# Optimization experiments

Hardware: AMD Instinct MI355X
Metric: run time of the kernel (lower is better)

Reference implementation:

```python
import jax, jax.numpy as jnp
import numpy as np

H = 8          # num_heads
WIN = 63       # win_size
LEFT = WIN - 1 - WIN // 2  # 31
EPS = 1e-5


def layer_norm(x, w, b):
    mu = x.mean(-1, keepdims=True)
    var = ((x - mu) ** 2).mean(-1, keepdims=True)
    return (x - mu) / jnp.sqrt(var + EPS) * w + b


def setup_inputs() -> dict:
    key = jax.random.key(0)
    N, T, C = 2, 2048, 512
    hid = 4 * C
    ks = jax.random.split(key, 16)
    s = 0.02
    return {
        "x": jax.random.normal(ks[0], (N, T, C), jnp.float32),
        "norm1_w": jnp.ones((C,), jnp.float32),
        "norm1_b": jnp.zeros((C,), jnp.float32),
        "qkv_w": jax.random.normal(ks[1], (3 * C, C), jnp.float32) * s,
        "qkv_b": jnp.zeros((3 * C,), jnp.float32),
        "rel_bias": jax.random.normal(ks[2], (H, WIN), jnp.float32) * s,
        "proj_w": jax.random.normal(ks[3], (C, C), jnp.float32) * s,
        "proj_b": jnp.zeros((C,), jnp.float32),
        "norm2_w": jnp.ones((C,), jnp.float32),
        "norm2_b": jnp.zeros((C,), jnp.float32),
        "fc1_w": jax.random.normal(ks[4], (hid, C), jnp.float32) * s,
        "fc1_b": jnp.zeros((hid,), jnp.float32),
        "fc2_w": jax.random.normal(ks[5], (C, hid), jnp.float32) * s,
        "fc2_b": jnp.zeros((C,), jnp.float32),
    }


def reference(x, norm1_w, norm1_b, qkv_w, qkv_b, rel_bias, proj_w, proj_b,
              norm2_w, norm2_b, fc1_w, fc1_b, fc2_w, fc2_b):
    N, T, C = x.shape
    hd = C // H
    scale = hd ** -0.5
    right = WIN - LEFT - 1

    shortcut = x
    h = layer_norm(x, norm1_w, norm1_b)
    qkv = (h @ qkv_w.T + qkv_b).reshape(N, T, 3, H, hd)
    q, k, v = qkv[:, :, 0], qkv[:, :, 1], qkv[:, :, 2]  # (N,T,H,hd)

    # zero-pad keys/values along time, gather sliding windows
    kp = jnp.pad(k, ((0, 0), (LEFT, right), (0, 0), (0, 0)))
    vp = jnp.pad(v, ((0, 0), (LEFT, right), (0, 0), (0, 0)))
    idx = jnp.arange(T)[:, None] + jnp.arange(WIN)[None, :]
    k_win = kp[:, idx]
    v_win = vp[:, idx]

    attn = jnp.einsum('nthd,ntwhd->nhtw', q * scale, k_win)
    attn = attn + rel_bias[None, :, None, :]
    # boundary mask: key position j = t - LEFT + w must lie in [0, T)
    pos = idx - LEFT
    mask = jnp.where((pos < 0) | (pos >= T), jnp.float32(-100.0), jnp.float32(0.0))
    attn = attn + mask[None, None, :, :]
    attn = jax.nn.softmax(attn, axis=-1)

    out = jnp.einsum('nhtw,ntwhd->nthd', attn, v_win).reshape(N, T, C)
    out = out @ proj_w.T + proj_b

    x = shortcut + out
    h2 = layer_norm(x, norm2_w, norm2_b)
    m = jax.nn.gelu(h2 @ fc1_w.T + fc1_b, approximate=False)  # torch nn.GELU = exact erf
    m = m @ fc2_w.T + fc2_b
    return x + m
```

## Files before the change

### kernel.cpp

```cpp
#include <hip/hip_runtime.h>

typedef unsigned short u16;
typedef unsigned int uint;
typedef __attribute__((ext_vector_type(4))) float floatx4;
typedef __attribute__((ext_vector_type(16))) float floatx16;
typedef __attribute__((ext_vector_type(8))) short shortx8;

__device__ __forceinline__ u16 f2b(float f) {
    unsigned int u = __float_as_uint(f);
    unsigned int r = (u + 0x7fffu + ((u >> 16) & 1u)) >> 16;
    return (u16)r;
}
__device__ __forceinline__ float b2f(u16 u) {
    return __uint_as_float(((unsigned int)u) << 16);
}
__device__ __forceinline__ void gl_lds16(const u16* g, u16* l) {
    __builtin_amdgcn_global_load_lds(
        (const __attribute__((address_space(1))) void*)g,
        (__attribute__((address_space(3))) void*)l, 16, 0, 0);
}
__device__ __forceinline__ float gelu_f(float v) {
    float e = __expf(1.59576912f * v * (1.0f + 0.044715f * v * v));
    return v * e / (e + 1.0f);
}

__device__ __forceinline__ void ln_row(const float* __restrict__ x,
                                       const float* __restrict__ w,
                                       const float* __restrict__ b,
                                       u16* __restrict__ out, int row,
                                       float* red) {
    const float2* xr = (const float2*)(x + (size_t)row * 512);
    float2 v = xr[threadIdx.x];
    float s = v.x + v.y;
    float s2 = v.x * v.x + v.y * v.y;
    #pragma unroll
    for (int o = 32; o > 0; o >>= 1) {
        s += __shfl_down(s, o, 64);
        s2 += __shfl_down(s2, o, 64);
    }
    int wid = threadIdx.x >> 6, lane = threadIdx.x & 63;
    if (lane == 0) { red[wid] = s; red[4 + wid] = s2; }
    __syncthreads();
    s = red[0] + red[1] + red[2] + red[3];
    s2 = red[4] + red[5] + red[6] + red[7];
    float mu = s * (1.0f / 512.0f);
    float var = s2 * (1.0f / 512.0f) - mu * mu;
    float rstd = rsqrtf(var + 1e-5f);
    float2 wv = ((const float2*)w)[threadIdx.x];
    float2 bv = ((const float2*)b)[threadIdx.x];
    float o0 = (v.x - mu) * rstd * wv.x + bv.x;
    float o1 = (v.y - mu) * rstd * wv.y + bv.y;
    unsigned int pack = (unsigned)f2b(o0) | ((unsigned)f2b(o1) << 16);
    ((unsigned int*)(out + (size_t)row * 512))[threadIdx.x] = pack;
}

__global__ __launch_bounds__(256) void ln_kernel_b(const u16* __restrict__ x,
                                                   const float* __restrict__ w,
                                                   const float* __restrict__ b,
                                                   u16* __restrict__ out) {
    __shared__ float red[8];
    int row = blockIdx.x;
    uint pv = ((const uint*)(x + (size_t)row * 512))[threadIdx.x];
    float vx = b2f((u16)(pv & 0xffffu)), vy = b2f((u16)(pv >> 16));
    float s = vx + vy;
    float s2 = vx * vx + vy * vy;
    #pragma unroll
    for (int o = 32; o > 0; o >>= 1) {
        s += __shfl_down(s, o, 64);
        s2 += __shfl_down(s2, o, 64);
    }
    int wid = threadIdx.x >> 6, lane = threadIdx.x & 63;
    if (lane == 0) { red[wid] = s; red[4 + wid] = s2; }
    __syncthreads();
    s = red[0] + red[1] + red[2] + red[3];
    s2 = red[4] + red[5] + red[6] + red[7];
    float mu = s * (1.0f / 512.0f);
    float var = s2 * (1.0f / 512.0f) - mu * mu;
    float rstd = rsqrtf(var + 1e-5f);
    float2 wv = ((const float2*)w)[threadIdx.x];
    float2 bv = ((const float2*)b)[threadIdx.x];
    float o0 = (vx - mu) * rstd * wv.x + bv.x;
    float o1 = (vy - mu) * rstd * wv.y + bv.y;
    unsigned int pack = (unsigned)f2b(o0) | ((unsigned)f2b(o1) << 16);
    ((unsigned int*)(out + (size_t)row * 512))[threadIdx.x] = pack;
}

__global__ __launch_bounds__(256) void prep_kernel(
    const float* __restrict__ qkvw, u16* __restrict__ wq,
    const float* __restrict__ projw, u16* __restrict__ wp,
    const float* __restrict__ fc1w, u16* __restrict__ w1,
    const float* __restrict__ fc2w, u16* __restrict__ w2,
    const float* __restrict__ x, const float* __restrict__ n1w,
    const float* __restrict__ n1b, u16* __restrict__ hb) {
    __shared__ float red[8];
    int bi = blockIdx.x;
    if (bi < 3072) {
        const float* src;
        u16* dst;
        int i0;
        if (bi < 768)       { src = qkvw; dst = wq; i0 = bi; }
        else if (bi < 1024) { src = projw; dst = wp; i0 = bi - 768; }
        else if (bi < 2048) { src = fc1w; dst = w1; i0 = bi - 1024; }
        else                { src = fc2w; dst = w2; i0 = bi - 2048; }
        int i = i0 * 256 + threadIdx.x;
        float4 v = ((const float4*)src)[i];
        uint2 o;
        o.x = (unsigned)f2b(v.x) | ((unsigned)f2b(v.y) << 16);
        o.y = (unsigned)f2b(v.z) | ((unsigned)f2b(v.w) << 16);
        ((uint2*)dst)[i] = o;
    } else {
        ln_row(x, n1w, n1b, hb, bi - 3072, red);
    }
}

template <int BM, int BN, int BK, int EPI>
__global__ __launch_bounds__(256, 2) void gemm_lds(const u16* __restrict__ A,
                                                   const u16* __restrict__ W,
                                                   const float* __restrict__ bias,
                                                   const float* __restrict__ residF,
                                                   const u16* __restrict__ residB,
                                                   float* __restrict__ outF,
                                                   u16* __restrict__ outB,
                                                   int M, int Nn, int K) {
    constexpr int MI = BM / 2 / 32;
    constexpr int NI = BN / 2 / 32;
    constexpr int CPR = BK / 8;
    constexpr int KMSK = CPR - 1;
    constexpr int ACH = BM * CPR / 256;
    constexpr int BCH = BN * CPR / 256;
    __shared__ u16 a_s[2][BM * BK];
    __shared__ u16 b_s[2][BN * BK];

    int tid = threadIdx.x;
    int wid = tid >> 6, lane = tid & 63;
    int wm = wid >> 1, wn = wid & 1;
    int m_blk = blockIdx.y * BM;
    int n_blk = blockIdx.x * BN;
    int lr = lane & 31;
    int lk = lane >> 5;

    floatx16 acc[MI][NI];
    #pragma unroll
    for (int i = 0; i < MI; i++)
        #pragma unroll
        for (int j = 0; j < NI; j++)
            #pragma unroll
            for (int r = 0; r < 16; r++) acc[i][j][r] = 0.f;

    const u16* Ag = A + (size_t)m_blk * K;
    const u16* Wg = W + (size_t)n_blk * K;

    int arow[ACH], akc[ACH], brow[BCH], bkc[BCH];
    #pragma unroll
    for (int p = 0; p < ACH; p++) {
        int c = p * 256 + tid;
        arow[p] = c / CPR;
        akc[p] = (c & KMSK) ^ (arow[p] & KMSK);
    }
    #pragma unroll
    for (int p = 0; p < BCH; p++) {
        int c = p * 256 + tid;
        brow[p] = c / CPR;
        bkc[p] = (c & KMSK) ^ (brow[p] & KMSK);
    }

    auto stage = [&](int k0, int buf) {
        #pragma unroll
        for (int p = 0; p < ACH; p++)
            gl_lds16(Ag + (size_t)arow[p] * K + k0 + akc[p] * 8,
                     a_s[buf] + (p * 256 + tid) * 8);
        #pragma unroll
        for (int p = 0; p < BCH; p++)
            gl_lds16(Wg + (size_t)brow[p] * K + k0 + bkc[p] * 8,
                     b_s[buf] + (p * 256 + tid) * 8);
    };

    stage(0, 0);
    int nit = K / BK;
    for (int it = 0; it < nit; it++) {
        __syncthreads();
        if (it + 1 < nit) stage((it + 1) * BK, (it + 1) & 1);
        int cb = it & 1;
        #pragma unroll
        for (int s = 0; s < BK / 16; s++) {
            shortx8 af[MI], bf[NI];
            int kc = s * 2 + lk;
            #pragma unroll
            for (int i = 0; i < MI; i++) {
                int row = wm * (BM / 2) + i * 32 + lr;
                af[i] = *(const shortx8*)(a_s[cb] + (row * CPR + (kc ^ (row & KMSK))) * 8);
            }
            #pragma unroll
            for (int j = 0; j < NI; j++) {
                int row = wn * (BN / 2) + j * 32 + lr;
                bf[j] = *(const shortx8*)(b_s[cb] + (row * CPR + (kc ^ (row & KMSK))) * 8);
            }
            #pragma unroll
            for (int i = 0; i < MI; i++)
                #pragma unroll
                for (int j = 0; j < NI; j++)
                    acc[i][j] = __builtin_amdgcn_mfma_f32_32x32x16_bf16(
                        af[i], bf[j], acc[i][j], 0, 0, 0);
        }
    }

    int col_l = lane & 31;
    int row_q = 4 * (lane >> 5);
    #pragma unroll
    for (int nj = 0; nj < NI; nj++) {
        int col = n_blk + wn * (BN / 2) + nj * 32 + col_l;
        float bv = bias[col];
        #pragma unroll
        for (int mi = 0; mi < MI; mi++) {
            #pragma unroll
            for (int r = 0; r < 16; r++) {
                int row = m_blk + wm * (BM / 2) + mi * 32 + (r & 3) + 8 * (r >> 2) + row_q;
                size_t off = (size_t)row * Nn + col;
                float v = acc[mi][nj][r] + bv;
                if (EPI == 1) {
                    outB[off] = f2b(v + residF[off]);
                } else if (EPI == 2) {
                    outB[off] = f2b(gelu_f(v));
                } else if (EPI == 3) {
                    outF[off] = v + b2f(residB[off]);
                } else {
                    outB[off] = f2b(v);
                }
            }
        }
    }
}

__global__ __launch_bounds__(256) void attn_kernel(const u16* __restrict__ qkv,
                                                   const float* __restrict__ rel_bias,
                                                   u16* __restrict__ out) {
    __shared__ u16 k_s[128][72];
    __shared__ u16 v_t[64][152];
    __shared__ u16 p_s[4][16][104];
    __shared__ float s_bias[64];

    int bx = blockIdx.x;
    int n = bx >> 8;
    int h = (bx >> 5) & 7;
    int t0 = (bx & 31) << 6;
    int tid = threadIdx.x, wid = tid >> 6, lane = tid & 63;
    int col = lane & 15, rq = lane >> 4;

    const u16* qrow = qkv + (size_t)(n * 2048 + t0 + wid * 16 + col) * 1536 + h * 64 + rq * 8;
    shortx8 qf0 = *(const shortx8*)qrow;
    shortx8 qf1 = *(const shortx8*)(qrow + 32);

    if (tid < 63) s_bias[tid] = rel_bias[h * 63 + tid];
    if (tid == 63) s_bias[63] = 0.f;

    const uint* qkv_u = (const uint*)qkv;
    for (int idx = tid; idx < 128 * 32; idx += 256) {
        int row = idx >> 5, j = idx & 31;
        int pos = t0 - 31 + row;
        uint kv = 0;
        if (pos >= 0 && pos < 2048)
            kv = qkv_u[(size_t)(n * 2048 + pos) * 768 + 256 + h * 32 + j];
        *(uint*)&k_s[row][j * 2] = kv;
    }
    for (int idx = tid; idx < 144 * 32; idx += 256) {
        int row = idx >> 5, j = idx & 31;
        int pos = t0 - 31 + row;
        uint vv = 0;
        if (pos >= 0 && pos < 2048)
            vv = qkv_u[(size_t)(n * 2048 + pos) * 768 + 512 + h * 32 + j];
        v_t[2 * j][row] = (u16)(vv & 0xffffu);
        v_t[2 * j + 1][row] = (u16)(vv >> 16);
    }
    __syncthreads();

    floatx4 S[5];
    #pragma unroll
    for (int nt = 0; nt < 5; nt++) S[nt] = (floatx4){0.f, 0.f, 0.f, 0.f};
    #pragma unroll
    for (int nt = 0; nt < 5; nt++) {
        const u16* kb = &k_s[wid * 16 + nt * 16 + col][rq * 8];
        shortx8 b0 = *(const shortx8*)kb;
        shortx8 b1 = *(const shortx8*)(kb + 32);
        S[nt] = __builtin_amdgcn_mfma_f32_16x16x32_bf16(qf0, b0, S[nt], 0, 0, 0);
        S[nt] = __builtin_amdgcn_mfma_f32_16x16x32_bf16(qf1, b1, S[nt], 0, 0, 0);
    }

    #pragma unroll
    for (int r = 0; r < 4; r++) {
        int t_row = rq * 4 + r;
        float sc[5];
        float mx = -1e30f;
        #pragma unroll
        for (int nt = 0; nt < 5; nt++) {
            int w = nt * 16 + col - t_row;
            int pos_abs = t0 - 31 + wid * 16 + nt * 16 + col;
            float v;
            if (w < 0 || w > 62) {
                v = -1e30f;
            } else {
                v = S[nt][r] * 0.125f + s_bias[w];
                if (pos_abs < 0 || pos_abs >= 2048) v -= 100.f;
            }
            sc[nt] = v;
            mx = fmaxf(mx, v);
        }
        #pragma unroll
        for (int o = 1; o < 16; o <<= 1) mx = fmaxf(mx, __shfl_xor(mx, o, 64));
        float l = 0.f;
        #pragma unroll
        for (int nt = 0; nt < 5; nt++) {
            sc[nt] = __expf(sc[nt] - mx);
            l += sc[nt];
        }
        #pragma unroll
        for (int o = 1; o < 16; o <<= 1) l += __shfl_xor(l, o, 64);
        float inv = 1.0f / l;
        #pragma unroll
        for (int nt = 0; nt < 5; nt++)
            p_s[wid][t_row][nt * 16 + col] = f2b(sc[nt] * inv);
        p_s[wid][t_row][80 + col] = 0;
    }
    __syncthreads();

    floatx4 O[4];
    #pragma unroll
    for (int dt = 0; dt < 4; dt++) O[dt] = (floatx4){0.f, 0.f, 0.f, 0.f};
    const u16* pr = &p_s[wid][col][rq * 8];
    shortx8 a0 = *(const shortx8*)pr;
    shortx8 a1 = *(const shortx8*)(pr + 32);
    shortx8 a2 = *(const shortx8*)(pr + 64);
    #pragma unroll
    for (int dt = 0; dt < 4; dt++) {
        const u16* vb = &v_t[dt * 16 + col][wid * 16 + rq * 8];
        shortx8 b0 = *(const shortx8*)vb;
        shortx8 b1 = *(const shortx8*)(vb + 32);
        shortx8 b2 = *(const shortx8*)(vb + 64);
        O[dt] = __builtin_amdgcn_mfma_f32_16x16x32_bf16(a0, b0, O[dt], 0, 0, 0);
        O[dt] = __builtin_amdgcn_mfma_f32_16x16x32_bf16(a1, b1, O[dt], 0, 0, 0);
        O[dt] = __builtin_amdgcn_mfma_f32_16x16x32_bf16(a2, b2, O[dt], 0, 0, 0);
    }

    #pragma unroll
    for (int dt = 0; dt < 4; dt++) {
        #pragma unroll
        for (int r = 0; r < 4; r++) {
            int t_row = rq * 4 + r;
            out[(size_t)(n * 2048 + t0 + wid * 16 + t_row) * 512 + h * 64 + dt * 16 + col] =
                f2b(O[dt][r]);
        }
    }
}

extern "C" void kernel_launch(void* const* d_in, const int* in_sizes, int n_in,
                              void* d_out, int out_size, void* d_ws, size_t ws_size,
                              hipStream_t stream) {
    const float* x     = (const float*)d_in[0];
    const float* n1w   = (const float*)d_in[1];
    const float* n1b   = (const float*)d_in[2];
    const float* qkvw  = (const float*)d_in[3];
    const float* qkvbv = (const float*)d_in[4];
    const float* relb  = (const float*)d_in[5];
    const float* projw = (const float*)d_in[6];
    const float* projb = (const float*)d_in[7];
    const float* n2w   = (const float*)d_in[8];
    const float* n2b   = (const float*)d_in[9];
    const float* fc1w  = (const float*)d_in[10];
    const float* fc1b  = (const float*)d_in[11];
    const float* fc2w  = (const float*)d_in[12];
    const float* fc2b  = (const float*)d_in[13];
    float* out = (float*)d_out;

    char* p = (char*)d_ws;
    u16* wq   = (u16*)p;  p += (size_t)786432 * 2;
    u16* wp   = (u16*)p;  p += (size_t)262144 * 2;
    u16* w1   = (u16*)p;  p += (size_t)1048576 * 2;
    u16* w2   = (u16*)p;  p += (size_t)1048576 * 2;
    u16* hb   = (u16*)p;  p += (size_t)2097152 * 2;
    u16* qkvb = (u16*)p;  p += (size_t)6291456 * 2;
    u16* attb = (u16*)p;  p += (size_t)2097152 * 2;
    u16* x2b  = (u16*)p;  p += (size_t)2097152 * 2;
    u16* mb   = (u16*)p;  p += (size_t)8388608 * 2;

    prep_kernel<<<7168, 256, 0, stream>>>(qkvw, wq, projw, wp, fc1w, w1, fc2w, w2,
                                          x, n1w, n1b, hb);
    gemm_lds<128, 128, 64, 0><<<dim3(12, 32), 256, 0, stream>>>(
        hb, wq, qkvbv, nullptr, nullptr, nullptr, qkvb, 4096, 1536, 512);
    attn_kernel<<<512, 256, 0, stream>>>(qkvb, relb, attb);
    gemm_lds<64, 64, 128, 1><<<dim3(8, 64), 256, 0, stream>>>(
        attb, wp, projb, x, nullptr, nullptr, x2b, 4096, 512, 512);
    ln_kernel_b<<<4096, 256, 0, stream>>>(x2b, n2w, n2b, hb);
    gemm_lds<128, 128, 64, 2><<<dim3(16, 32), 256, 0, stream>>>(
        hb, w1, fc1b, nullptr, nullptr, nullptr, mb, 4096, 2048, 512);
    gemm_lds<64, 64, 128, 3><<<dim3(8, 64), 256, 0, stream>>>(
        mb, w2, fc2b, nullptr, x2b, out, nullptr, 4096, 512, 2048);
}
```

Before: 177.8 us.

## Use wave-per-row layernorm and split GEMMs into 16x16 and 32x32 MFMA variants

Layernorm kernels now process one row per wavefront with 128-bit loads and xor-shuffle reductions, which removes the LDS reduction and block barrier and cuts the block count. The large GEMMs (QKV, FC1) move to a dedicated kernel using 16x16x32 MFMA with a 4x4 accumulator tile per wave. The small-N GEMMs (proj, FC2) get a specialised single 32x32 accumulator kernel. Grid axes are swapped so consecutive blocks walk along M, which changes how blocks share weight tiles in cache.

Measured after the change: 167.6 us, median of 2. 5.7% less time.

```diff
diff --git a/kernel.cpp b/kernel.cpp
--- a/kernel.cpp
+++ b/kernel.cpp
@@ -24,65 +24,82 @@
     return v * e / (e + 1.0f);
 }
 
-__device__ __forceinline__ void ln_row(const float* __restrict__ x,
-                                       const float* __restrict__ w,
-                                       const float* __restrict__ b,
-                                       u16* __restrict__ out, int row,
-                                       float* red) {
-    const float2* xr = (const float2*)(x + (size_t)row * 512);
-    float2 v = xr[threadIdx.x];
-    float s = v.x + v.y;
-    float s2 = v.x * v.x + v.y * v.y;
+__device__ __forceinline__ void ln_row_wave_f32(const float* __restrict__ x,
+                                                const float* __restrict__ w,
+                                                const float* __restrict__ b,
+                                                u16* __restrict__ out, int row) {
+    int lane = threadIdx.x & 63;
+    const float4* xr = (const float4*)(x + (size_t)row * 512);
+    float4 v0 = xr[lane * 2], v1 = xr[lane * 2 + 1];
+    float s = v0.x + v0.y + v0.z + v0.w + v1.x + v1.y + v1.z + v1.w;
+    float s2 = v0.x * v0.x + v0.y * v0.y + v0.z * v0.z + v0.w * v0.w +
+               v1.x * v1.x + v1.y * v1.y + v1.z * v1.z + v1.w * v1.w;
     #pragma unroll
     for (int o = 32; o > 0; o >>= 1) {
-        s += __shfl_down(s, o, 64);
-        s2 += __shfl_down(s2, o, 64);
-    }
-    int wid = threadIdx.x >> 6, lane = threadIdx.x & 63;
-    if (lane == 0) { red[wid] = s; red[4 + wid] = s2; }
-    __syncthreads();
-    s = red[0] + red[1] + red[2] + red[3];
-    s2 = red[4] + red[5] + red[6] + red[7];
+        s += __shfl_xor(s, o, 64);
+        s2 += __shfl_xor(s2, o, 64);
+    }
     float mu = s * (1.0f / 512.0f);
     float var = s2 * (1.0f / 512.0f) - mu * mu;
     float rstd = rsqrtf(var + 1e-5f);
-    float2 wv = ((const float2*)w)[threadIdx.x];
-    float2 bv = ((const float2*)b)[threadIdx.x];
-    float o0 = (v.x - mu) * rstd * wv.x + bv.x;
-    float o1 = (v.y - mu) * rstd * wv.y + bv.y;
-    unsigned int pack = (unsigned)f2b(o0) | ((unsigned)f2b(o1) << 16);
-    ((unsigned int*)(out + (size_t)row * 512))[threadIdx.x] = pack;
+    const float4* wr = (const float4*)w;
+    const float4* br = (const float4*)b;
+    float4 w0 = wr[lane * 2], w1 = wr[lane * 2 + 1];
+    float4 b0 = br[lane * 2], b1 = br[lane * 2 + 1];
+    uint4 o4;
+    o4.x = (uint)f2b((v0.x - mu) * rstd * w0.x + b0.x) |
+           ((uint)f2b((v0.y - mu) * rstd * w0.y + b0.y) << 16);
+    o4.y = (uint)f2b((v0.z - mu) * rstd * w0.z + b0.z) |
+           ((uint)f2b((v0.w - mu) * rstd * w0.w + b0.w) << 16);
+    o4.z = (uint)f2b((v1.x - mu) * rstd * w1.x + b1.x) |
+           ((uint)f2b((v1.y - mu) * rstd * w1.y + b1.y) << 16);
+    o4.w = (uint)f2b((v1.z - mu) * rstd * w1.z + b1.z) |
+           ((uint)f2b((v1.w - mu) * rstd * w1.w + b1.w) << 16);
+    ((uint4*)(out + (size_t)row * 512))[lane] = o4;
 }
 
 __global__ __launch_bounds__(256) void ln_kernel_b(const u16* __restrict__ x,
                                                    const float* __restrict__ w,
                                                    const float* __restrict__ b,
                                                    u16* __restrict__ out) {
-    __shared__ float red[8];
-    int row = blockIdx.x;
-    uint pv = ((const uint*)(x + (size_t)row * 512))[threadIdx.x];
-    float vx = b2f((u16)(pv & 0xffffu)), vy = b2f((u16)(pv >> 16));
-    float s = vx + vy;
-    float s2 = vx * vx + vy * vy;
+    int row = blockIdx.x * 4 + (threadIdx.x >> 6);
+    int lane = threadIdx.x & 63;
+    uint4 p = ((const uint4*)(x + (size_t)row * 512))[lane];
+    float v[8];
+    v[0] = b2f((u16)(p.x & 0xffffu)); v[1] = b2f((u16)(p.x >> 16));
+    v[2] = b2f((u16)(p.y & 0xffffu)); v[3] = b2f((u16)(p.y >> 16));
+    v[4] = b2f((u16)(p.z & 0xffffu)); v[5] = b2f((u16)(p.z >> 16));
+    v[6] = b2f((u16)(p.w & 0xffffu)); v[7] = b2f((u16)(p.w >> 16));
+    float s = 0.f, s2 = 0.f;
+    #pragma unroll
+    for (int i = 0; i < 8; i++) { s += v[i]; s2 += v[i] * v[i]; }
     #pragma unroll
     for (int o = 32; o > 0; o >>= 1) {
-        s += __shfl_down(s, o, 64);
-        s2 += __shfl_down(s2, o, 64);
-    }
-    int wid = threadIdx.x >> 6, lane = threadIdx.x & 63;
-    if (lane == 0) { red[wid] = s; red[4 + wid] = s2; }
-    __syncthreads();
-    s = red[0] + red[1] + red[2] + red[3];
-    s2 = red[4] + red[5] + red[6] + red[7];
+        s += __shfl_xor(s, o, 64);
+        s2 += __shfl_xor(s2, o, 64);
+    }
     float mu = s * (1.0f / 512.0f);
     float var = s2 * (1.0f / 512.0f) - mu * mu;
     float rstd = rsqrtf(var + 1e-5f);
-    float2 wv = ((const float2*)w)[threadIdx.x];
-    float2 bv = ((const float2*)b)[threadIdx.x];
-    float o0 = (vx - mu) * rstd * wv.x + bv.x;
-    float o1 = (vy - mu) * rstd * wv.y + bv.y;
-    unsigned int pack = (unsigned)f2b(o0) | ((unsigned)f2b(o1) << 16);
-    ((unsigned int*)(out + (size_t)row * 512))[threadIdx.x] = pack;
+    const float4* wr = (const float4*)w;
+    const float4* br = (const float4*)b;
+    float4 w0 = wr[lane * 2], w1 = wr[lane * 2 + 1];
+    float4 b0 = br[lane * 2], b1 = br[lane * 2 + 1];
+    float o8[8];
+    o8[0] = (v[0] - mu) * rstd * w0.x + b0.x;
+    o8[1] = (v[1] - mu) * rstd * w0.y + b0.y;
+    o8[2] = (v[2] - mu) * rstd * w0.z + b0.z;
+    o8[3] = (v[3] - mu) * rstd * w0.w + b0.w;
+    o8[4] = (v[4] - mu) * rstd * w1.x + b1.x;
+    o8[5] = (v[5] - mu) * rstd * w1.y + b1.y;
+    o8[6] = (v[6] - mu) * rstd * w1.z + b1.z;
+    o8[7] = (v[7] - mu) * rstd * w1.w + b1.w;
+    uint4 o4;
+    o4.x = (uint)f2b(o8[0]) | ((uint)f2b(o8[1]) << 16);
+    o4.y = (uint)f2b(o8[2]) | ((uint)f2b(o8[3]) << 16);
+    o4.z = (uint)f2b(o8[4]) | ((uint)f2b(o8[5]) << 16);
+    o4.w = (uint)f2b(o8[6]) | ((uint)f2b(o8[7]) << 16);
+    ((uint4*)(out + (size_t)row * 512))[lane] = o4;
 }
 
 __global__ __launch_bounds__(256) void prep_kernel(
@@ -92,7 +109,6 @@
     const float* __restrict__ fc2w, u16* __restrict__ w2,
     const float* __restrict__ x, const float* __restrict__ n1w,
     const float* __restrict__ n1b, u16* __restrict__ hb) {
-    __shared__ float red[8];
     int bi = blockIdx.x;
     if (bi < 3072) {
         const float* src;
@@ -105,73 +121,144 @@
         int i = i0 * 256 + threadIdx.x;
         float4 v = ((const float4*)src)[i];
         uint2 o;
-        o.x = (unsigned)f2b(v.x) | ((unsigned)f2b(v.y) << 16);
-        o.y = (unsigned)f2b(v.z) | ((unsigned)f2b(v.w) << 16);
+        o.x = (uint)f2b(v.x) | ((uint)f2b(v.y) << 16);
+        o.y = (uint)f2b(v.z) | ((uint)f2b(v.w) << 16);
         ((uint2*)dst)[i] = o;
     } else {
-        ln_row(x, n1w, n1b, hb, bi - 3072, red);
-    }
-}
-
-template <int BM, int BN, int BK, int EPI>
-__global__ __launch_bounds__(256, 2) void gemm_lds(const u16* __restrict__ A,
-                                                   const u16* __restrict__ W,
-                                                   const float* __restrict__ bias,
-                                                   const float* __restrict__ residF,
-                                                   const u16* __restrict__ residB,
-                                                   float* __restrict__ outF,
-                                                   u16* __restrict__ outB,
-                                                   int M, int Nn, int K) {
-    constexpr int MI = BM / 2 / 32;
-    constexpr int NI = BN / 2 / 32;
-    constexpr int CPR = BK / 8;
-    constexpr int KMSK = CPR - 1;
-    constexpr int ACH = BM * CPR / 256;
-    constexpr int BCH = BN * CPR / 256;
+        int row = (bi - 3072) * 4 + (threadIdx.x >> 6);
+        ln_row_wave_f32(x, n1w, n1b, hb, row);
+    }
+}
+
+template <int EPI>
+__global__ __launch_bounds__(256, 2) void gemm16(const u16* __restrict__ A,
+                                                 const u16* __restrict__ W,
+                                                 const float* __restrict__ bias,
+                                                 u16* __restrict__ outB,
+                                                 int M, int Nn, int K) {
+    constexpr int BM = 128, BN = 128, BK = 64;
     __shared__ u16 a_s[2][BM * BK];
     __shared__ u16 b_s[2][BN * BK];
 
     int tid = threadIdx.x;
     int wid = tid >> 6, lane = tid & 63;
     int wm = wid >> 1, wn = wid & 1;
-    int m_blk = blockIdx.y * BM;
-    int n_blk = blockIdx.x * BN;
+    int m_blk = blockIdx.x * BM;
+    int n_blk = blockIdx.y * BN;
+    int lr = lane & 15;
+    int lkc = lane >> 4;
+
+    floatx4 acc[4][4];
+    #pragma unroll
+    for (int i = 0; i < 4; i++)
+        #pragma unroll
+        for (int j = 0; j < 4; j++) acc[i][j] = (floatx4){0.f, 0.f, 0.f, 0.f};
+
+    const u16* Ag = A + (size_t)m_blk * K;
+    const u16* Wg = W + (size_t)n_blk * K;
+
+    int srow = tid >> 3;
+    int skc = (tid & 7) ^ (srow & 7);
+
+    auto stage = [&](int k0, int buf) {
+        #pragma unroll
+        for (int p = 0; p < 4; p++)
+            gl_lds16(Ag + (size_t)(p * 32 + srow) * K + k0 + skc * 8,
+                     a_s[buf] + (p * 256 + tid) * 8);
+        #pragma unroll
+        for (int p = 0; p < 4; p++)
+            gl_lds16(Wg + (size_t)(p * 32 + srow) * K + k0 + skc * 8,
+                     b_s[buf] + (p * 256 + tid) * 8);
+    };
+
+    stage(0, 0);
+    int nit = K >> 6;
+    for (int it = 0; it < nit; it++) {
+        __syncthreads();
+        if (it + 1 < nit) stage((it + 1) << 6, (it + 1) & 1);
+        int cb = it & 1;
+        #pragma unroll
+        for (int s = 0; s < 2; s++) {
+            int kc = s * 4 + lkc;
+            shortx8 af[4], bf[4];
+            #pragma unroll
+            for (int i = 0; i < 4; i++) {
+                int row = wm * 64 + i * 16 + lr;
+                af[i] = *(const shortx8*)(a_s[cb] + (row * 8 + (kc ^ (row & 7))) * 8);
+            }
+            #pragma unroll
+            for (int j = 0; j < 4; j++) {
+                int row = wn * 64 + j * 16 + lr;
+                bf[j] = *(const shortx8*)(b_s[cb] + (row * 8 + (kc ^ (row & 7))) * 8);
+            }
+            #pragma unroll
+            for (int i = 0; i < 4; i++)
+                #pragma unroll
+                for (int j = 0; j < 4; j++)
+                    acc[i][j] = __builtin_amdgcn_mfma_f32_16x16x32_bf16(
+                        af[i], bf[j], acc[i][j], 0, 0, 0);
+        }
+    }
+
+    int col_l = lane & 15;
+    int row_base = (lane >> 4) * 4;
+    #pragma unroll
+    for (int nj = 0; nj < 4; nj++) {
+        int col = n_blk + wn * 64 + nj * 16 + col_l;
+        float bv = bias[col];
+        #pragma unroll
+        for (int mi = 0; mi < 4; mi++) {
+            #pragma unroll
+            for (int r = 0; r < 4; r++) {
+                int row = m_blk + wm * 64 + mi * 16 + row_base + r;
+                size_t off = (size_t)row * Nn + col;
+                float v = acc[mi][nj][r] + bv;
+                outB[off] = f2b(EPI == 2 ? gelu_f(v) : v);
+            }
+        }
+    }
+}
+
+template <int EPI>
+__global__ __launch_bounds__(256, 2) void gemm32(const u16* __restrict__ A,
+                                                 const u16* __restrict__ W,
+                                                 const float* __restrict__ bias,
+                                                 const float* __restrict__ residF,
+                                                 const u16* __restrict__ residB,
+                                                 float* __restrict__ outF,
+                                                 u16* __restrict__ outB,
+                                                 int M, int Nn, int K) {
+    constexpr int BM = 64, BN = 64, BK = 128;
+    constexpr int CPR = BK / 8, KMSK = CPR - 1;
+    __shared__ u16 a_s[2][BM * BK];
+    __shared__ u16 b_s[2][BN * BK];
+
+    int tid = threadIdx.x;
+    int wid = tid >> 6, lane = tid & 63;
+    int wm = wid >> 1, wn = wid & 1;
+    int m_blk = blockIdx.x * BM;
+    int n_blk = blockIdx.y * BN;
     int lr = lane & 31;
     int lk = lane >> 5;
 
-    floatx16 acc[MI][NI];
-    #pragma unroll
-    for (int i = 0; i < MI; i++)
-        #pragma unroll
-        for (int j = 0; j < NI; j++)
-            #pragma unroll
-            for (int r = 0; r < 16; r++) acc[i][j][r] = 0.f;
+    floatx16 acc;
+    #pragma unroll
+    for (int r = 0; r < 16; r++) acc[r] = 0.f;
 
     const u16* Ag = A + (size_t)m_blk * K;
     const u16* Wg = W + (size_t)n_blk * K;
 
-    int arow[ACH], akc[ACH], brow[BCH], bkc[BCH];
-    #pragma unroll
-    for (int p = 0; p < ACH; p++) {
-        int c = p * 256 + tid;
-        arow[p] = c / CPR;
-        akc[p] = (c & KMSK) ^ (arow[p] & KMSK);
-    }
-    #pragma unroll
-    for (int p = 0; p < BCH; p++) {
-        int c = p * 256 + tid;
-        brow[p] = c / CPR;
-        bkc[p] = (c & KMSK) ^ (brow[p] & KMSK);
-    }
+    int srow = tid / CPR;
+    int skc = (tid & KMSK) ^ (srow & KMSK);
 
     auto stage = [&](int k0, int buf) {
         #pragma unroll
-        for (int p = 0; p < ACH; p++)
-            gl_lds16(Ag + (size_t)arow[p] * K + k0 + akc[p] * 8,
+        for (int p = 0; p < 4; p++)
+            gl_lds16(Ag + (size_t)(p * 16 + srow) * K + k0 + skc * 8,
                      a_s[buf] + (p * 256 + tid) * 8);
         #pragma unroll
-        for (int p = 0; p < BCH; p++)
-            gl_lds16(Wg + (size_t)brow[p] * K + k0 + bkc[p] * 8,
+        for (int p = 0; p < 4; p++)
+            gl_lds16(Wg + (size_t)(p * 16 + srow) * K + k0 + skc * 8,
                      b_s[buf] + (p * 256 + tid) * 8);
     };
 
@@ -183,51 +270,26 @@
         int cb = it & 1;
         #pragma unroll
         for (int s = 0; s < BK / 16; s++) {
-            shortx8 af[MI], bf[NI];
             int kc = s * 2 + lk;
-            #pragma unroll
-            for (int i = 0; i < MI; i++) {
-                int row = wm * (BM / 2) + i * 32 + lr;
-                af[i] = *(const shortx8*)(a_s[cb] + (row * CPR + (kc ^ (row & KMSK))) * 8);
-            }
-            #pragma unroll
-            for (int j = 0; j < NI; j++) {
-                int row = wn * (BN / 2) + j * 32 + lr;
-                bf[j] = *(const shortx8*)(b_s[cb] + (row * CPR + (kc ^ (row & KMSK))) * 8);
-            }
-            #pragma unroll
-            for (int i = 0; i < MI; i++)
-                #pragma unroll
-                for (int j = 0; j < NI; j++)
-                    acc[i][j] = __builtin_amdgcn_mfma_f32_32x32x16_bf16(
-                        af[i], bf[j], acc[i][j], 0, 0, 0);
+            int arow = wm * 32 + lr;
+            int brow = wn * 32 + lr;
+            shortx8 af = *(const shortx8*)(a_s[cb] + (arow * CPR + (kc ^ (arow & KMSK))) * 8);
+            shortx8 bf = *(const shortx8*)(b_s[cb] + (brow * CPR + (kc ^ (brow & KMSK))) * 8);
+            acc = __builtin_amdgcn_mfma_f32_32x32x16_bf16(af, bf, acc, 0, 0, 0);
         }
     }
 
     int col_l = lane & 31;
     int row_q = 4 * (lane >> 5);
-    #pragma unroll
-    for (int nj = 0; nj < NI; nj++) {
-        int col = n_blk + wn * (BN / 2) + nj * 32 + col_l;
-        float bv = bias[col];
-        #pragma unroll
-        for (int mi = 0; mi < MI; mi++) {
-            #pragma unroll
-            for (int r = 0; r < 16; r++) {
-                int row = m_blk + wm * (BM / 2) + mi * 32 + (r & 3) + 8 * (r >> 2) + row_q;
-                size_t off = (size_t)row * Nn + col;
-                float v = acc[mi][nj][r] + bv;
-                if (EPI == 1) {
-                    outB[off] = f2b(v + residF[off]);
-                } else if (EPI == 2) {
-                    outB[off] = f2b(gelu_f(v));
-                } else if (EPI == 3) {
-                    outF[off] = v + b2f(residB[off]);
-                } else {
-                    outB[off] = f2b(v);
-                }
-            }
-        }
+    int col = n_blk + wn * 32 + col_l;
+    float bv = bias[col];
+    #pragma unroll
+    for (int r = 0; r < 16; r++) {
+        int row = m_blk + wm * 32 + (r & 3) + 8 * (r >> 2) + row_q;
+        size_t off = (size_t)row * Nn + col;
+        float v = acc[r] + bv;
+        if (EPI == 1) outB[off] = f2b(v + residF[off]);
+        else          outF[off] = v + b2f(residB[off]);
     }
 }
 
@@ -381,16 +443,14 @@
     u16* x2b  = (u16*)p;  p += (size_t)2097152 * 2;
     u16* mb   = (u16*)p;  p += (size_t)8388608 * 2;
 
-    prep_kernel<<<7168, 256, 0, stream>>>(qkvw, wq, projw, wp, fc1w, w1, fc2w, w2,
+    prep_kernel<<<4096, 256, 0, stream>>>(qkvw, wq, projw, wp, fc1w, w1, fc2w, w2,
                                           x, n1w, n1b, hb);
-    gemm_lds<128, 128, 64, 0><<<dim3(12, 32), 256, 0, stream>>>(
-        hb, wq, qkvbv, nullptr, nullptr, nullptr, qkvb, 4096, 1536, 512);
+    gemm16<0><<<dim3(32, 12), 256, 0, stream>>>(hb, wq, qkvbv, qkvb, 4096, 1536, 512);
     attn_kernel<<<512, 256, 0, stream>>>(qkvb, relb, attb);
-    gemm_lds<64, 64, 128, 1><<<dim3(8, 64), 256, 0, stream>>>(
-        attb, wp, projb, x, nullptr, nullptr, x2b, 4096, 512, 512);
-    ln_kernel_b<<<4096, 256, 0, stream>>>(x2b, n2w, n2b, hb);
-    gemm_lds<128, 128, 64, 2><<<dim3(16, 32), 256, 0, stream>>>(
-        hb, w1, fc1b, nullptr, nullptr, nullptr, mb, 4096, 2048, 512);
-    gemm_lds<64, 64, 128, 3><<<dim3(8, 64), 256, 0, stream>>>(
-        mb, w2, fc2b, nullptr, x2b, out, nullptr, 4096, 512, 2048);
-}
+    gemm32<1><<<dim3(64, 8), 256, 0, stream>>>(attb, wp, projb, x, nullptr,
+                                               nullptr, x2b, 4096, 512, 512);
+    ln_kernel_b<<<1024, 256, 0, stream>>>(x2b, n2w, n2b, hb);
+    gemm16<2><<<dim3(32, 16), 256, 0, stream>>>(hb, w1, fc1b, mb, 4096, 2048, 512);
+    gemm32<3><<<dim3(64, 8), 256, 0, stream>>>(mb, w2, fc2b, nullptr, x2b,
+                                               out, nullptr, 4096, 512, 2048);
+}
```
